# Kernel tuning notes

Measured on AMD Instinct MI355X. Metric: run time of the kernel, lower is better.

## Reference

```python
import jax, jax.numpy as jnp
import numpy as np

B, T, N, K = 1024, 4096, 2048, 16
M = 1 << K  # per-neuron memory size (use_hashing=False -> 2**k)


def setup_inputs() -> dict:
    key = jax.random.key(0)
    k1, k2, k3 = jax.random.split(key, 3)
    input_bits = jax.random.randint(k1, (B, T), 0, 2, dtype=jnp.int32)          # 0/1 bits
    connections = jax.random.randint(k2, (N, K), 0, T, dtype=jnp.int32)         # fixed wiring
    memory = jax.random.randint(k3, (N, M), 0, 256, dtype=jnp.int32)            # per-neuron RAM contents
    return {"input_bits": input_bits, "connections": connections, "memory": memory}


def reference(input_bits, connections, memory):
    # gather the k wired bits for every neuron: [B, N, K]
    gathered = input_bits[:, connections].astype(jnp.int32)
    # bit weights = powers of two (RAMNeuron._bit_weights), LSB-first
    bit_weights = (jnp.int32(1) << jnp.arange(K, dtype=jnp.int32))              # [K]
    # weighted sum -> memory address per (sample, neuron): [B, N]
    addresses = jnp.sum(gathered * bit_weights, axis=-1)
    # per-neuron memory lookup: memory[n, addresses[b, n]] -> [B, N]
    mems = memory[jnp.arange(N)[None, :], addresses]
    # output is the stored LSB as a bool bit
    return (mems & 1).astype(jnp.bool_)
```

## Files before the change

### kernel.cpp

```cpp
#include <hip/hip_runtime.h>
#include <cstdint>

#define Bc 1024
#define Tc 4096
#define Nc 2048
#define Kc 16
#define Mc 65536

#define PACK_GRID 2048
#define PACK_BLK  256

__global__ __launch_bounds__(PACK_BLK) void pack_bit0(
    const int* __restrict__ memory,
    unsigned long long* __restrict__ packed)
{
    const int tid  = threadIdx.x;
    const int lane = tid & 63;
    const size_t stride = (size_t)PACK_GRID * PACK_BLK;
    size_t base = (size_t)blockIdx.x * PACK_BLK + tid;

    for (int it = 0; it < 256 / 8; ++it) {
        int v[8];
#pragma unroll
        for (int j = 0; j < 8; ++j)
            v[j] = memory[base + (size_t)j * stride];
#pragma unroll
        for (int j = 0; j < 8; ++j) {
            const unsigned long long m = __ballot(v[j] & 1);
            if (lane == 0) {
                packed[(base + (size_t)j * stride) >> 6] = m;
            }
        }
        base += 8 * stride;
    }
}

__global__ __launch_bounds__(256) void ram_lookup_packed(
    const int* __restrict__ input_bits,
    const int* __restrict__ connections,
    const uint32_t* __restrict__ packed,
    int* __restrict__ out)
{
    __shared__ uint32_t bits[Tc / 32];

    const int b    = blockIdx.x;
    const int tid  = threadIdx.x;
    const int lane = tid & 63;
    const int wave = tid >> 6;

    const int* row = input_bits + (size_t)b * Tc;

#pragma unroll
    for (int i = 0; i < Tc / 256; ++i) {
        const int pos = i * 256 + wave * 64 + lane;
        const unsigned long long m = __ballot(row[pos] & 1);
        if (lane == 0) {
            const int w64 = i * 4 + wave;
            bits[w64 * 2]     = (uint32_t)m;
            bits[w64 * 2 + 1] = (uint32_t)(m >> 32);
        }
    }
    __syncthreads();

    int vals[Nc / 256];
#pragma unroll
    for (int i = 0; i < Nc / 256; ++i) {
        const int n = i * 256 + tid;
        const int4* cp = (const int4*)(connections + n * Kc);
        const int4 c0 = cp[0], c1 = cp[1], c2 = cp[2], c3 = cp[3];
        const int c[16] = {c0.x, c0.y, c0.z, c0.w,
                           c1.x, c1.y, c1.z, c1.w,
                           c2.x, c2.y, c2.z, c2.w,
                           c3.x, c3.y, c3.z, c3.w};
        uint32_t a = 0;
#pragma unroll
        for (int k = 0; k < 16; ++k) {
            const uint32_t t = (uint32_t)c[k];
            a |= ((bits[t >> 5] >> (t & 31)) & 1u) << k;
        }
        const uint32_t w = packed[((uint32_t)n << 11) + (a >> 5)];
        vals[i] = (int)((w >> (a & 31)) & 1u);
    }

#pragma unroll
    for (int i = 0; i < Nc / 256; ++i) {
        out[(size_t)b * Nc + i * 256 + tid] = vals[i];
    }
}

__global__ __launch_bounds__(256) void ram_lookup_fused(
    const int* __restrict__ input_bits,
    const int* __restrict__ connections,
    const int* __restrict__ memory,
    int* __restrict__ out)
{
    __shared__ uint32_t bits[Tc / 32];

    const int b    = blockIdx.x;
    const int tid  = threadIdx.x;
    const int lane = tid & 63;
    const int wave = tid >> 6;

    const int* row = input_bits + (size_t)b * Tc;

#pragma unroll
    for (int i = 0; i < Tc / 256; ++i) {
        const int pos = i * 256 + wave * 64 + lane;
        const unsigned long long m = __ballot(row[pos] & 1);
        if (lane == 0) {
            const int w64 = i * 4 + wave;
            bits[w64 * 2]     = (uint32_t)m;
            bits[w64 * 2 + 1] = (uint32_t)(m >> 32);
        }
    }
    __syncthreads();

    int vals[Nc / 256];
#pragma unroll
    for (int i = 0; i < Nc / 256; ++i) {
        const int n = i * 256 + tid;
        const int4* cp = (const int4*)(connections + n * Kc);
        const int4 c0 = cp[0], c1 = cp[1], c2 = cp[2], c3 = cp[3];
        const int c[16] = {c0.x, c0.y, c0.z, c0.w,
                           c1.x, c1.y, c1.z, c1.w,
                           c2.x, c2.y, c2.z, c2.w,
                           c3.x, c3.y, c3.z, c3.w};
        uint32_t a = 0;
#pragma unroll
        for (int k = 0; k < 16; ++k) {
            const uint32_t t = (uint32_t)c[k];
            a |= ((bits[t >> 5] >> (t & 31)) & 1u) << k;
        }
        vals[i] = memory[((size_t)n << 16) + a];
    }

#pragma unroll
    for (int i = 0; i < Nc / 256; ++i) {
        out[(size_t)b * Nc + i * 256 + tid] = vals[i] & 1;
    }
}

extern "C" void kernel_launch(void* const* d_in, const int* in_sizes, int n_in,
                              void* d_out, int out_size, void* d_ws, size_t ws_size,
                              hipStream_t stream) {
    const int* input_bits  = (const int*)d_in[0];
    const int* connections = (const int*)d_in[1];
    const int* memory      = (const int*)d_in[2];
    int* out               = (int*)d_out;

    const size_t packed_bytes = (size_t)Nc * Mc / 8;

    if (ws_size >= packed_bytes) {
        unsigned long long* pk64 = (unsigned long long*)d_ws;
        hipLaunchKernelGGL(pack_bit0, dim3(PACK_GRID), dim3(PACK_BLK), 0, stream,
                           memory, pk64);
        hipLaunchKernelGGL(ram_lookup_packed, dim3(Bc), dim3(256), 0, stream,
                           input_bits, connections, (const uint32_t*)pk64, out);
    } else {
        hipLaunchKernelGGL(ram_lookup_fused, dim3(Bc), dim3(256), 0, stream,
                           input_bits, connections, memory, out);
    }
}
```

Before: 740.8 us.

## Pack memory LSBs with 16-byte vector loads and permuted bit layout

The packing kernel now reads the 512MB memory table with int4 vector loads instead of scalar loads. Each thread handles four consecutive entries, so the bitmasks come out in a permuted order, and the lookup kernel's address math is rewritten to match that layout. The aim is to cut load instruction count and raise bandwidth efficiency in the dominant memory scan. In exchange, lookups use more index arithmetic and each 256-entry chunk is stored interleaved across 8 words.

```diff
diff --git a/kernel.cpp b/kernel.cpp
--- a/kernel.cpp
+++ b/kernel.cpp
@@ -7,31 +7,43 @@
 #define Kc 16
 #define Mc 65536
 
-#define PACK_GRID 2048
-#define PACK_BLK  256
+#define SCAN_GRID 2048
+#define SCAN_BLK  256
 
-__global__ __launch_bounds__(PACK_BLK) void pack_bit0(
+typedef int v4i __attribute__((ext_vector_type(4)));
+
+__global__ __launch_bounds__(SCAN_BLK) void pack_bit0_v4(
     const int* __restrict__ memory,
-    unsigned long long* __restrict__ packed)
+    uint32_t* __restrict__ packed)
 {
     const int tid  = threadIdx.x;
     const int lane = tid & 63;
-    const size_t stride = (size_t)PACK_GRID * PACK_BLK;
-    size_t base = (size_t)blockIdx.x * PACK_BLK + tid;
+    const size_t g      = (size_t)blockIdx.x * SCAN_BLK + tid;
+    const size_t stride = (size_t)SCAN_GRID * SCAN_BLK;
+    const v4i* src = (const v4i*)memory;
 
-    for (int it = 0; it < 256 / 8; ++it) {
-        int v[8];
-#pragma unroll
-        for (int j = 0; j < 8; ++j)
-            v[j] = memory[base + (size_t)j * stride];
+    for (int it = 0; it < 8; ++it) {
+        v4i v[8];
+        size_t idx[8];
 #pragma unroll
         for (int j = 0; j < 8; ++j) {
-            const unsigned long long m = __ballot(v[j] & 1);
-            if (lane == 0) {
-                packed[(base + (size_t)j * stride) >> 6] = m;
+            idx[j] = (size_t)(it * 8 + j) * stride + g;
+            v[j] = src[idx[j]];
+        }
+#pragma unroll
+        for (int j = 0; j < 8; ++j) {
+            const unsigned long long m0 = __ballot(v[j].x & 1);
+            const unsigned long long m1 = __ballot(v[j].y & 1);
+            const unsigned long long m2 = __ballot(v[j].z & 1);
+            const unsigned long long m3 = __ballot(v[j].w & 1);
+            if (lane < 8) {
+                const int c = lane >> 1;
+                const unsigned long long mm =
+                    (c == 0) ? m0 : (c == 1) ? m1 : (c == 2) ? m2 : m3;
+                const size_t q = (idx[j] - lane) >> 6;
+                packed[q * 8 + lane] = (uint32_t)(mm >> ((lane & 1) << 5));
             }
         }
-        base += 8 * stride;
     }
 }
 
@@ -78,8 +90,9 @@
             const uint32_t t = (uint32_t)c[k];
             a |= ((bits[t >> 5] >> (t & 31)) & 1u) << k;
         }
-        const uint32_t w = packed[((uint32_t)n << 11) + (a >> 5)];
-        vals[i] = (int)((w >> (a & 31)) & 1u);
+        const uint32_t widx = ((uint32_t)n << 11)
+                            + ((a >> 8) << 3) + ((a & 3) << 1) + ((a >> 7) & 1);
+        vals[i] = (int)((packed[widx] >> ((a >> 2) & 31)) & 1u);
     }
 
 #pragma unroll
@@ -151,11 +164,11 @@
     const size_t packed_bytes = (size_t)Nc * Mc / 8;
 
     if (ws_size >= packed_bytes) {
-        unsigned long long* pk64 = (unsigned long long*)d_ws;
-        hipLaunchKernelGGL(pack_bit0, dim3(PACK_GRID), dim3(PACK_BLK), 0, stream,
-                           memory, pk64);
+        uint32_t* packed = (uint32_t*)d_ws;
+        hipLaunchKernelGGL(pack_bit0_v4, dim3(SCAN_GRID), dim3(SCAN_BLK), 0, stream,
+                           memory, packed);
         hipLaunchKernelGGL(ram_lookup_packed, dim3(Bc), dim3(256), 0, stream,
-                           input_bits, connections, (const uint32_t*)pk64, out);
+                           input_bits, connections, packed, out);
     } else {
         hipLaunchKernelGGL(ram_lookup_fused, dim3(Bc), dim3(256), 0, stream,
                            input_bits, connections, memory, out);
```

Result: no change. 738.2 us (-0.4%).
